# Optimization experiments

Measured on AMD Instinct MI355X. Metric: run time of the kernel, lower is better.

Reference implementation:

```python
import jax, jax.numpy as jnp
import numpy as np

NEG_BIG = -9.0e15


def masked_mean_softmax(idx):
    # softmax over a 0/-inf mask == uniform weights over positions where idx > 0
    logits = jnp.where(idx > 0, 1.0, NEG_BIG).astype(jnp.float32)
    return jax.nn.softmax(logits, axis=1)


def setup_inputs() -> dict:
    key = jax.random.key(0)
    ks = jax.random.split(key, 8)
    N_NODES, N_EDGES, EDGE_ARITY, NODE_DEG = 100000, 50000, 32, 16
    D_IN, D_OUT, TV = 128, 128, 128
    stdv = 1.0 / np.sqrt(D_IN)
    u = lambda k, shp: jax.random.uniform(k, shp, jnp.float32, -stdv, stdv)
    return {
        "x": jax.random.normal(ks[0], (N_NODES, D_IN), jnp.float32),
        "seq": jax.random.randint(ks[1], (N_EDGES, EDGE_ARITY), 0, N_NODES),
        "useq": jax.random.randint(ks[2], (N_NODES, NODE_DEG), 0, N_EDGES),
        "TextVector": jax.random.normal(ks[3], (TV,), jnp.float32),
        "weight1": u(ks[4], (D_IN, D_OUT)),
        "weight2": u(ks[5], (D_OUT, D_OUT)),
        "weight3": u(ks[6], (TV, TV)),
    }


def reference(x, seq, useq, TextVector, weight1, weight2, weight3):
    # NOTE: the torch module overwrites TextVector with weight3[0]; dropout is
    # a no-op in eval mode and is omitted here.
    tv = weight3[0]                                   # [TV]
    dot = weight3 @ tv                                # [TV]
    cos = dot / (jnp.linalg.norm(tv) * jnp.linalg.norm(weight3, axis=1))
    inter_nw = jnp.mean(cos)                          # scalar

    xw = (x @ weight1) * inter_nw                     # [N, D_OUT]

    nor = masked_mean_softmax(seq)                    # [E, A]
    adj_with_fea = xw[seq]                            # [E, A, D_OUT] gather
    edge = jnp.einsum('eac,ea->ec', adj_with_fea, nor)
    edge = jax.nn.relu(edge)
    e1 = edge @ weight2                               # [E, D_OUT]

    u_nor = masked_mean_softmax(useq)                 # [N, K]
    edge_adj = e1[useq]                               # [N, K, D_OUT] gather
    node = jnp.einsum('nkc,nk->nc', edge_adj, u_nor)  # [N, D_OUT]
    return node
```

## Files before the change

### kernel.cpp

```cpp
#include <hip/hip_runtime.h>
#include <hip/hip_fp16.h>

#define ND 100000
#define NE 50000
#define AR 32
#define DG 16
#define D  128

typedef _Float16 half8_t __attribute__((ext_vector_type(8)));
typedef _Float16 half4_t __attribute__((ext_vector_type(4)));
typedef float    f32x4_t __attribute__((ext_vector_type(4)));

#define APAD 136
#define EPB 128

__global__ __launch_bounds__(256) void k_prep(const float* __restrict__ w1,
                                              const float* __restrict__ w2,
                                              const float* __restrict__ w3,
                                              _Float16* __restrict__ w1f,
                                              _Float16* __restrict__ w2f,
                                              float* __restrict__ inter_out) {
    if (blockIdx.x == 64) {
        __shared__ float red[128];
        int j = threadIdx.x;
        if (j < 128) {
            float dot = 0.f, sq = 0.f, sq0 = 0.f;
            #pragma unroll 8
            for (int k = 0; k < D; ++k) {
                float wj = w3[j * D + k];
                float w0 = w3[k];
                dot += wj * w0;
                sq  += wj * wj;
                sq0 += w0 * w0;
            }
            red[j] = dot / (sqrtf(sq0) * sqrtf(sq));
        }
        __syncthreads();
        if (j == 0) {
            float s = 0.f;
            for (int i = 0; i < 128; ++i) s += red[i];
            inter_out[0] = s / 128.f;
        }
        return;
    }
    int o = blockIdx.x * 256 + threadIdx.x;
    int j    = o & 7;
    int lane = (o >> 3) & 63;
    int frag = o >> 9;
    int ntile = frag >> 2, ktile = frag & 3;
    int n = ntile * 16 + (lane & 15);
    int k = ktile * 32 + (lane >> 4) * 8 + j;
    w1f[o] = (_Float16)w1[k * D + n];
    w2f[o] = (_Float16)w2[k * D + n];
}

__global__ __launch_bounds__(256) void k_xw(const float* __restrict__ x,
                                            const _Float16* __restrict__ w1f_g,
                                            const float* __restrict__ inter_p,
                                            _Float16* __restrict__ xws) {
    __shared__ _Float16 wfrag[D * D];
    __shared__ _Float16 xs[64 * APAD];
    int t = threadIdx.x;
    {
        const float4* src = (const float4*)w1f_g;
        float4* dst = (float4*)wfrag;
        #pragma unroll
        for (int i = 0; i < 8; ++i) dst[i * 256 + t] = src[i * 256 + t];
    }
    int rowbase = blockIdx.x * 64;
    #pragma unroll
    for (int p = 0; p < 8; ++p) {
        int idx = p * 1024 + t * 4;
        int r = idx >> 7, c = idx & 127;
        int grow = rowbase + r;
        float4 v = make_float4(0.f, 0.f, 0.f, 0.f);
        if (grow < ND) v = ((const float4*)x)[(size_t)grow * 32 + (c >> 2)];
        half4_t h = { (_Float16)v.x, (_Float16)v.y, (_Float16)v.z, (_Float16)v.w };
        *(half4_t*)&xs[r * APAD + c] = h;
    }
    __syncthreads();

    int wave = t >> 6, lane = t & 63;
    int quad = lane >> 4, l15 = lane & 15;
    int m0 = wave * 16;
    float inter = inter_p[0];

    half8_t a[4];
    #pragma unroll
    for (int kt = 0; kt < 4; ++kt)
        a[kt] = *(const half8_t*)&xs[(m0 + l15) * APAD + kt * 32 + quad * 8];

    int grow = rowbase + m0 + l15;
    #pragma unroll
    for (int nt = 0; nt < 8; ++nt) {
        f32x4_t acc = {0.f, 0.f, 0.f, 0.f};
        #pragma unroll
        for (int kt = 0; kt < 4; ++kt) {
            half8_t b = *(const half8_t*)&wfrag[((nt * 4 + kt) * 64 + lane) * 8];
            acc = __builtin_amdgcn_mfma_f32_16x16x32_f16(b, a[kt], acc, 0, 0, 0);
        }
        half4_t hv = { (_Float16)(acc[0] * inter), (_Float16)(acc[1] * inter),
                       (_Float16)(acc[2] * inter), (_Float16)(acc[3] * inter) };
        if (grow < ND)
            *(half4_t*)(xws + ((size_t)nt * ND + grow) * 16 + quad * 4) = hv;
    }
}

__global__ __launch_bounds__(256, 4) void k_gather_e(const int* __restrict__ seq,
                                                     const _Float16* __restrict__ xws,
                                                     _Float16* __restrict__ ea) {
    int t = threadIdx.x;
    int s = blockIdx.x & 7;
    int g = blockIdx.x >> 3;
    int e = t >> 1, part = t & 1;
    int eg = g * EPB + e;
    int egs = min(eg, NE - 1);

    const int4* sp = (const int4*)(seq + (size_t)egs * AR);
    int4 q0 = sp[0], q1 = sp[1], q2 = sp[2], q3 = sp[3];
    int4 q4 = sp[4], q5 = sp[5], q6 = sp[6], q7 = sp[7];
    int idxs[32] = { q0.x, q0.y, q0.z, q0.w, q1.x, q1.y, q1.z, q1.w,
                     q2.x, q2.y, q2.z, q2.w, q3.x, q3.y, q3.z, q3.w,
                     q4.x, q4.y, q4.z, q4.w, q5.x, q5.y, q5.z, q5.w,
                     q6.x, q6.y, q6.z, q6.w, q7.x, q7.y, q7.z, q7.w };
    int cnt = 0;
    #pragma unroll
    for (int j = 0; j < AR; ++j) cnt += (idxs[j] > 0);
    bool allv = (cnt == 0);
    float wv = 1.f / (float)(allv ? AR : cnt);

    const _Float16* tab = xws + (size_t)s * ND * 16 + part * 8;

    float acc[8] = {};
    #pragma unroll
    for (int tt = 0; tt < AR; ++tt) {
        int ix = idxs[tt];
        float w = (allv | (ix > 0)) ? wv : 0.f;
        half8_t v = *(const half8_t*)(tab + (size_t)ix * 16);
        #pragma unroll
        for (int jj = 0; jj < 8; ++jj)
            acc[jj] = fmaf(w, (float)v[jj], acc[jj]);
    }
    if (eg < NE) {
        half8_t h;
        #pragma unroll
        for (int jj = 0; jj < 8; ++jj) h[jj] = (_Float16)fmaxf(acc[jj], 0.f);
        *(half8_t*)(ea + (size_t)eg * D + s * 16 + part * 8) = h;
    }
}

__global__ __launch_bounds__(256) void k_gemm_e(const _Float16* __restrict__ ea,
                                                const _Float16* __restrict__ w2f_g,
                                                _Float16* __restrict__ e1s) {
    __shared__ _Float16 wfrag[D * D];
    __shared__ _Float16 et[64 * APAD];
    int t = threadIdx.x;
    {
        const float4* src = (const float4*)w2f_g;
        float4* dst = (float4*)wfrag;
        #pragma unroll
        for (int i = 0; i < 8; ++i) dst[i * 256 + t] = src[i * 256 + t];
    }
    int rowbase = blockIdx.x * 64;
    #pragma unroll
    for (int p = 0; p < 4; ++p) {
        int hidx = p * 2048 + t * 8;
        int r = hidx >> 7, c = hidx & 127;
        int grow = rowbase + r;
        int gs = (grow < NE) ? grow : (NE - 1);
        half8_t v = *(const half8_t*)(ea + (size_t)gs * D + c);
        *(half8_t*)&et[r * APAD + c] = v;
    }
    __syncthreads();

    int wave = t >> 6, lane = t & 63;
    int quad = lane >> 4, l15 = lane & 15;
    int m0 = wave * 16;

    half8_t a[4];
    #pragma unroll
    for (int kt = 0; kt < 4; ++kt)
        a[kt] = *(const half8_t*)&et[(m0 + l15) * APAD + kt * 32 + quad * 8];

    int grow = rowbase + m0 + l15;
    #pragma unroll
    for (int nt = 0; nt < 8; ++nt) {
        f32x4_t acc = {0.f, 0.f, 0.f, 0.f};
        #pragma unroll
        for (int kt = 0; kt < 4; ++kt) {
            half8_t b = *(const half8_t*)&wfrag[((nt * 4 + kt) * 64 + lane) * 8];
            acc = __builtin_amdgcn_mfma_f32_16x16x32_f16(b, a[kt], acc, 0, 0, 0);
        }
        half4_t hv = { (_Float16)acc[0], (_Float16)acc[1],
                       (_Float16)acc[2], (_Float16)acc[3] };
        if (grow < NE)
            *(half4_t*)(e1s + ((size_t)(nt >> 1) * NE + grow) * 32
                            + (nt & 1) * 16 + quad * 4) = hv;
    }
}

__global__ __launch_bounds__(256, 4) void k_gather_n(const int* __restrict__ useq,
                                                     const _Float16* __restrict__ e1s,
                                                     float* __restrict__ out) {
    int t = threadIdx.x;
    int s = blockIdx.x & 3;
    int g = blockIdx.x >> 2;
    int n = t >> 2, part = t & 3;
    int ng = g * 64 + n;
    int ns = min(ng, ND - 1);

    const int4* up = (const int4*)(useq + (size_t)ns * DG);
    int4 q0 = up[0], q1 = up[1], q2 = up[2], q3 = up[3];
    int idxs[16] = { q0.x, q0.y, q0.z, q0.w, q1.x, q1.y, q1.z, q1.w,
                     q2.x, q2.y, q2.z, q2.w, q3.x, q3.y, q3.z, q3.w };
    int cnt = 0;
    #pragma unroll
    for (int j = 0; j < DG; ++j) cnt += (idxs[j] > 0);
    bool allv = (cnt == 0);
    float wv = 1.f / (float)(allv ? DG : cnt);

    const _Float16* tab = e1s + (size_t)s * NE * 32 + part * 8;

    float acc[8] = {};
    #pragma unroll
    for (int tt = 0; tt < DG; ++tt) {
        int ix = idxs[tt];
        float w = (allv | (ix > 0)) ? wv : 0.f;
        half8_t v = *(const half8_t*)(tab + (size_t)ix * 32);
        #pragma unroll
        for (int jj = 0; jj < 8; ++jj)
            acc[jj] = fmaf(w, (float)v[jj], acc[jj]);
    }
    if (ng < ND) {
        f32x4_t o0 = { acc[0], acc[1], acc[2], acc[3] };
        f32x4_t o1 = { acc[4], acc[5], acc[6], acc[7] };
        f32x4_t* p = (f32x4_t*)(out + (size_t)ng * D + s * 32 + part * 8);
        __builtin_nontemporal_store(o0, p);
        __builtin_nontemporal_store(o1, p + 1);
    }
}

extern "C" void kernel_launch(void* const* d_in, const int* in_sizes, int n_in,
                              void* d_out, int out_size, void* d_ws, size_t ws_size,
                              hipStream_t stream) {
    const float* x    = (const float*)d_in[0];
    const int*   seq  = (const int*)d_in[1];
    const int*   useq = (const int*)d_in[2];
    const float* w1   = (const float*)d_in[4];
    const float* w2   = (const float*)d_in[5];
    const float* w3   = (const float*)d_in[6];
    float* out = (float*)d_out;

    _Float16* xws   = (_Float16*)d_out;
    _Float16* ea    = (_Float16*)d_out + (size_t)ND * D;
    float*    inter = (float*)d_ws;
    _Float16* w1f   = (_Float16*)((char*)d_ws + 256);
    _Float16* w2f   = (_Float16*)((char*)d_ws + 256 + 32768);
    _Float16* e1s   = (_Float16*)((char*)d_ws + 256 + 65536);

    int eg_grp = (NE + EPB - 1) / EPB;
    int ng_grp = (ND + 63) / 64;

    hipLaunchKernelGGL(k_prep,     dim3(65),             dim3(256), 0, stream, w1, w2, w3, w1f, w2f, inter);
    hipLaunchKernelGGL(k_xw,       dim3((ND + 63) / 64), dim3(256), 0, stream, x, w1f, inter, xws);
    hipLaunchKernelGGL(k_gather_e, dim3(eg_grp * 8),     dim3(256), 0, stream, seq, xws, ea);
    hipLaunchKernelGGL(k_gemm_e,   dim3((NE + 63) / 64), dim3(256), 0, stream, ea, w2f, e1s);
    hipLaunchKernelGGL(k_gather_n, dim3(ng_grp * 4),     dim3(256), 0, stream, useq, e1s, out);
}
```

Measured before the change: 231.2 us.

## Widen xw slices to 64B, batch gather loads, add nontemporal hints

The xw table layout changes from 8 slices of 16 halves (32B rows) to 4 slices of 32 halves (64B rows). The edge gather now uses 4 threads per edge over 64 edges per block and 4 slices, matching the node-gather structure. This halves how often seq indices are reloaded across slices and makes each random gather fetch a 64B row instead of 32B. Both gather loops issue four independent row loads before accumulating, to raise memory-level parallelism. Nontemporal loads and stores are added for the index arrays and intermediate outputs. The trade-off is a larger per-slice table working set (about 6.4MB per slice), which may reduce cache hit rates.

```diff
diff --git a/kernel.cpp b/kernel.cpp
--- a/kernel.cpp
+++ b/kernel.cpp
@@ -10,9 +10,9 @@
 typedef _Float16 half8_t __attribute__((ext_vector_type(8)));
 typedef _Float16 half4_t __attribute__((ext_vector_type(4)));
 typedef float    f32x4_t __attribute__((ext_vector_type(4)));
+typedef int      i32x4_t __attribute__((ext_vector_type(4)));
 
 #define APAD 136
-#define EPB 128
 
 __global__ __launch_bounds__(256) void k_prep(const float* __restrict__ w1,
                                               const float* __restrict__ w2,
@@ -101,8 +101,11 @@
         }
         half4_t hv = { (_Float16)(acc[0] * inter), (_Float16)(acc[1] * inter),
                        (_Float16)(acc[2] * inter), (_Float16)(acc[3] * inter) };
-        if (grow < ND)
-            *(half4_t*)(xws + ((size_t)nt * ND + grow) * 16 + quad * 4) = hv;
+        if (grow < ND) {
+            half4_t* dst = (half4_t*)(xws + ((size_t)(nt >> 1) * ND + grow) * 32
+                                          + (nt & 1) * 16 + quad * 4);
+            __builtin_nontemporal_store(hv, dst);
+        }
     }
 }
 
@@ -110,42 +113,59 @@
                                                      const _Float16* __restrict__ xws,
                                                      _Float16* __restrict__ ea) {
     int t = threadIdx.x;
-    int s = blockIdx.x & 7;
-    int g = blockIdx.x >> 3;
-    int e = t >> 1, part = t & 1;
-    int eg = g * EPB + e;
+    int s = blockIdx.x & 3;
+    int g = blockIdx.x >> 2;
+    int e = t >> 2, part = t & 3;
+    int eg = g * 64 + e;
     int egs = min(eg, NE - 1);
 
-    const int4* sp = (const int4*)(seq + (size_t)egs * AR);
-    int4 q0 = sp[0], q1 = sp[1], q2 = sp[2], q3 = sp[3];
-    int4 q4 = sp[4], q5 = sp[5], q6 = sp[6], q7 = sp[7];
-    int idxs[32] = { q0.x, q0.y, q0.z, q0.w, q1.x, q1.y, q1.z, q1.w,
-                     q2.x, q2.y, q2.z, q2.w, q3.x, q3.y, q3.z, q3.w,
-                     q4.x, q4.y, q4.z, q4.w, q5.x, q5.y, q5.z, q5.w,
-                     q6.x, q6.y, q6.z, q6.w, q7.x, q7.y, q7.z, q7.w };
+    const i32x4_t* sp = (const i32x4_t*)(seq + (size_t)egs * AR);
+    i32x4_t q0 = __builtin_nontemporal_load(sp + 0);
+    i32x4_t q1 = __builtin_nontemporal_load(sp + 1);
+    i32x4_t q2 = __builtin_nontemporal_load(sp + 2);
+    i32x4_t q3 = __builtin_nontemporal_load(sp + 3);
+    i32x4_t q4 = __builtin_nontemporal_load(sp + 4);
+    i32x4_t q5 = __builtin_nontemporal_load(sp + 5);
+    i32x4_t q6 = __builtin_nontemporal_load(sp + 6);
+    i32x4_t q7 = __builtin_nontemporal_load(sp + 7);
+    int idxs[32] = { q0[0], q0[1], q0[2], q0[3], q1[0], q1[1], q1[2], q1[3],
+                     q2[0], q2[1], q2[2], q2[3], q3[0], q3[1], q3[2], q3[3],
+                     q4[0], q4[1], q4[2], q4[3], q5[0], q5[1], q5[2], q5[3],
+                     q6[0], q6[1], q6[2], q6[3], q7[0], q7[1], q7[2], q7[3] };
     int cnt = 0;
     #pragma unroll
     for (int j = 0; j < AR; ++j) cnt += (idxs[j] > 0);
     bool allv = (cnt == 0);
     float wv = 1.f / (float)(allv ? AR : cnt);
 
-    const _Float16* tab = xws + (size_t)s * ND * 16 + part * 8;
+    const _Float16* tab = xws + (size_t)s * ND * 32 + part * 8;
 
     float acc[8] = {};
     #pragma unroll
-    for (int tt = 0; tt < AR; ++tt) {
-        int ix = idxs[tt];
-        float w = (allv | (ix > 0)) ? wv : 0.f;
-        half8_t v = *(const half8_t*)(tab + (size_t)ix * 16);
-        #pragma unroll
-        for (int jj = 0; jj < 8; ++jj)
-            acc[jj] = fmaf(w, (float)v[jj], acc[jj]);
+    for (int gq = 0; gq < 8; ++gq) {
+        int i0 = idxs[gq * 4 + 0], i1 = idxs[gq * 4 + 1];
+        int i2 = idxs[gq * 4 + 2], i3 = idxs[gq * 4 + 3];
+        half8_t v0 = *(const half8_t*)(tab + (size_t)i0 * 32);
+        half8_t v1 = *(const half8_t*)(tab + (size_t)i1 * 32);
+        half8_t v2 = *(const half8_t*)(tab + (size_t)i2 * 32);
+        half8_t v3 = *(const half8_t*)(tab + (size_t)i3 * 32);
+        float w0 = (allv | (i0 > 0)) ? wv : 0.f;
+        float w1 = (allv | (i1 > 0)) ? wv : 0.f;
+        float w2 = (allv | (i2 > 0)) ? wv : 0.f;
+        float w3 = (allv | (i3 > 0)) ? wv : 0.f;
+        #pragma unroll
+        for (int jj = 0; jj < 8; ++jj) {
+            acc[jj] = fmaf(w0, (float)v0[jj], acc[jj]);
+            acc[jj] = fmaf(w1, (float)v1[jj], acc[jj]);
+            acc[jj] = fmaf(w2, (float)v2[jj], acc[jj]);
+            acc[jj] = fmaf(w3, (float)v3[jj], acc[jj]);
+        }
     }
     if (eg < NE) {
         half8_t h;
         #pragma unroll
         for (int jj = 0; jj < 8; ++jj) h[jj] = (_Float16)fmaxf(acc[jj], 0.f);
-        *(half8_t*)(ea + (size_t)eg * D + s * 16 + part * 8) = h;
+        __builtin_nontemporal_store(h, (half8_t*)(ea + (size_t)eg * D + s * 32 + part * 8));
     }
 }
 
@@ -209,10 +229,13 @@
     int ng = g * 64 + n;
     int ns = min(ng, ND - 1);
 
-    const int4* up = (const int4*)(useq + (size_t)ns * DG);
-    int4 q0 = up[0], q1 = up[1], q2 = up[2], q3 = up[3];
-    int idxs[16] = { q0.x, q0.y, q0.z, q0.w, q1.x, q1.y, q1.z, q1.w,
-                     q2.x, q2.y, q2.z, q2.w, q3.x, q3.y, q3.z, q3.w };
+    const i32x4_t* up = (const i32x4_t*)(useq + (size_t)ns * DG);
+    i32x4_t q0 = __builtin_nontemporal_load(up + 0);
+    i32x4_t q1 = __builtin_nontemporal_load(up + 1);
+    i32x4_t q2 = __builtin_nontemporal_load(up + 2);
+    i32x4_t q3 = __builtin_nontemporal_load(up + 3);
+    int idxs[16] = { q0[0], q0[1], q0[2], q0[3], q1[0], q1[1], q1[2], q1[3],
+                     q2[0], q2[1], q2[2], q2[3], q3[0], q3[1], q3[2], q3[3] };
     int cnt = 0;
     #pragma unroll
     for (int j = 0; j < DG; ++j) cnt += (idxs[j] > 0);
@@ -223,13 +246,24 @@
 
     float acc[8] = {};
     #pragma unroll
-    for (int tt = 0; tt < DG; ++tt) {
-        int ix = idxs[tt];
-        float w = (allv | (ix > 0)) ? wv : 0.f;
-        half8_t v = *(const half8_t*)(tab + (size_t)ix * 32);
-        #pragma unroll
-        for (int jj = 0; jj < 8; ++jj)
-            acc[jj] = fmaf(w, (float)v[jj], acc[jj]);
+    for (int gq = 0; gq < 4; ++gq) {
+        int i0 = idxs[gq * 4 + 0], i1 = idxs[gq * 4 + 1];
+        int i2 = idxs[gq * 4 + 2], i3 = idxs[gq * 4 + 3];
+        half8_t v0 = *(const half8_t*)(tab + (size_t)i0 * 32);
+        half8_t v1 = *(const half8_t*)(tab + (size_t)i1 * 32);
+        half8_t v2 = *(const half8_t*)(tab + (size_t)i2 * 32);
+        half8_t v3 = *(const half8_t*)(tab + (size_t)i3 * 32);
+        float w0 = (allv | (i0 > 0)) ? wv : 0.f;
+        float w1 = (allv | (i1 > 0)) ? wv : 0.f;
+        float w2 = (allv | (i2 > 0)) ? wv : 0.f;
+        float w3 = (allv | (i3 > 0)) ? wv : 0.f;
+        #pragma unroll
+        for (int jj = 0; jj < 8; ++jj) {
+            acc[jj] = fmaf(w0, (float)v0[jj], acc[jj]);
+            acc[jj] = fmaf(w1, (float)v1[jj], acc[jj]);
+            acc[jj] = fmaf(w2, (float)v2[jj], acc[jj]);
+            acc[jj] = fmaf(w3, (float)v3[jj], acc[jj]);
+        }
     }
     if (ng < ND) {
         f32x4_t o0 = { acc[0], acc[1], acc[2], acc[3] };
@@ -258,12 +292,12 @@
     _Float16* w2f   = (_Float16*)((char*)d_ws + 256 + 32768);
     _Float16* e1s   = (_Float16*)((char*)d_ws + 256 + 65536);
 
-    int eg_grp = (NE + EPB - 1) / EPB;
+    int eg_grp = (NE + 63) / 64;
     int ng_grp = (ND + 63) / 64;
 
     hipLaunchKernelGGL(k_prep,     dim3(65),             dim3(256), 0, stream, w1, w2, w3, w1f, w2f, inter);
     hipLaunchKernelGGL(k_xw,       dim3((ND + 63) / 64), dim3(256), 0, stream, x, w1f, inter, xws);
-    hipLaunchKernelGGL(k_gather_e, dim3(eg_grp * 8),     dim3(256), 0, stream, seq, xws, ea);
+    hipLaunchKernelGGL(k_gather_e, dim3(eg_grp * 4),     dim3(256), 0, stream, seq, xws, ea);
     hipLaunchKernelGGL(k_gemm_e,   dim3((NE + 63) / 64), dim3(256), 0, stream, ea, w2f, e1s);
     hipLaunchKernelGGL(k_gather_n, dim3(ng_grp * 4),     dim3(256), 0, stream, useq, e1s, out);
 }
```

Result: slower. 243.9 us (+5.5%).
